# Performance work log

Measured on AMD Instinct MI355X. Metric: run time of the kernel, lower is better.

The kernel has to match this reference:

```python
import jax, jax.numpy as jnp
import numpy as np
from jax import lax

NUM_HEADS = 8
EMBED_DIM = 256
KEY_DIM = EMBED_DIM // NUM_HEADS  # 32


def rotate_every_two(x):
    x1 = x[..., ::2]
    x2 = x[..., 1::2]
    return jnp.stack((-x2, x1), axis=-1).reshape(x.shape)


def theta_shift(x, sin, cos):
    return x * cos + rotate_every_two(x) * sin


def setup_inputs() -> dict:
    key = jax.random.key(0)
    ks = jax.random.split(key, 16)
    b, H, W, E = 16, 64, 64, EMBED_DIM
    kd = KEY_DIM
    gain = 2 ** (-2.5)
    std_proj = gain * (2.0 / (E + E)) ** 0.5  # xavier_normal with gain
    std_out = (2.0 / (E + E)) ** 0.5
    return {
        "x": jax.random.normal(ks[0], (b, H, W, E), jnp.float32),
        "sin": jax.random.normal(ks[1], (H, W, kd), jnp.float32),
        "cos": jax.random.normal(ks[2], (H, W, kd), jnp.float32),
        "mask_h": jax.random.normal(ks[3], (NUM_HEADS, H, H), jnp.float32),
        "mask_w": jax.random.normal(ks[4], (NUM_HEADS, W, W), jnp.float32),
        "q_w": jax.random.normal(ks[5], (E, E), jnp.float32) * std_proj,
        "q_b": jnp.zeros((E,), jnp.float32),
        "k_w": jax.random.normal(ks[6], (E, E), jnp.float32) * std_proj,
        "k_b": jnp.zeros((E,), jnp.float32),
        "v_w": jax.random.normal(ks[7], (E, E), jnp.float32) * std_proj,
        "v_b": jnp.zeros((E,), jnp.float32),
        "lepe_w": jax.random.normal(ks[8], (5, 5, 1, E), jnp.float32) * 0.05,  # HWIO depthwise
        "lepe_b": jnp.zeros((E,), jnp.float32),
        "out_w": jax.random.normal(ks[9], (E, E), jnp.float32) * std_out,
        "out_b": jnp.zeros((E,), jnp.float32),
    }


def reference(x, sin, cos, mask_h, mask_w, q_w, q_b, k_w, k_b, v_w, v_b,
              lepe_w, lepe_b, out_w, out_b):
    b, H, W, E = x.shape
    nH, kd = NUM_HEADS, KEY_DIM
    vd = E // nH
    scaling = kd ** (-0.5)

    q = x @ q_w + q_b                       # [b,H,W,E]
    k = (x @ k_w + k_b) * scaling
    v = x @ v_w + v_b

    # depthwise 5x5 conv (lepe), NHWC
    lepe = lax.conv_general_dilated(
        v, lepe_w, window_strides=(1, 1), padding=[(2, 2), (2, 2)],
        dimension_numbers=("NHWC", "HWIO", "NHWC"), feature_group_count=E) + lepe_b

    q = q.reshape(b, H, W, nH, kd)
    k = k.reshape(b, H, W, nH, kd)
    v = v.reshape(b, H, W, nH, vd)

    sin_b = sin[:, :, None, :]              # [H,W,1,kd]
    cos_b = cos[:, :, None, :]
    qr = theta_shift(q, sin_b, cos_b)       # [b,H,W,nH,kd]
    kr = theta_shift(k, sin_b, cos_b)

    # width-wise attention: scores [b,H,nH,W,W]
    qk_w = jnp.einsum("bhqnd,bhknd->bhnqk", qr, kr)
    attn_w = jax.nn.softmax(qk_w + mask_w[None, None], axis=-1)
    v1 = jnp.einsum("bhnqk,bhknd->bhqnd", attn_w, v)  # [b,H,W,nH,vd]

    # height-wise attention: scores [b,W,nH,H,H]
    qk_h = jnp.einsum("bqwnd,bkwnd->bwnqk", qr, kr)
    attn_h = jax.nn.softmax(qk_h + mask_h[None, None], axis=-1)
    out = jnp.einsum("bwnqk,bkwnd->bqwnd", attn_h, v1)  # [b,H,W,nH,vd]

    out = out.reshape(b, H, W, E) + lepe
    return out @ out_w + out_b
```

## Files before the change

kernel.cpp:

```cpp
#include <hip/hip_runtime.h>

typedef unsigned short u16;
typedef __attribute__((ext_vector_type(4))) float f32x4;
typedef __attribute__((ext_vector_type(8))) short bf16x8;
typedef __attribute__((ext_vector_type(8))) u16 u16x8;
typedef __attribute__((ext_vector_type(4))) u16 u16x4v;

#define DI __device__ __forceinline__

DI u16 f2bf(float f) {
  unsigned int x = __float_as_uint(f);
  unsigned int r = (x + 0x7fffu + ((x >> 16) & 1u)) >> 16;
  return (u16)r;
}
DI float bf2f(u16 u) { return __uint_as_float(((unsigned int)u) << 16); }

__global__ __launch_bounds__(256) void pack_kernel(
    const float* __restrict__ qw, const float* __restrict__ qb,
    const float* __restrict__ kw, const float* __restrict__ kb,
    const float* __restrict__ vw, const float* __restrict__ vb,
    const float* __restrict__ ow,
    u16* __restrict__ wqkvT, float* __restrict__ bias, u16* __restrict__ owT)
{
  const int r = blockIdx.x;
  const int t = threadIdx.x;
  if (r < 768) {
    const int p = r >> 8, c = r & 255;
    const float* wsrc = p == 0 ? qw : (p == 1 ? kw : vw);
    const float sc = (p == 1) ? 0.17677669529663687f : 1.0f;
    wqkvT[r * 256 + t] = f2bf(wsrc[t * 256 + c] * sc);
    if (t == 0) {
      const float* bs = p == 0 ? qb : (p == 1 ? kb : vb);
      bias[r] = bs[c] * sc;
    }
  } else {
    const int c = r - 768;
    owT[c * 256 + t] = f2bf(ow[t * 256 + c]);
  }
}

__global__ __launch_bounds__(256, 6) void qkv_gemm_kernel(
    const float* __restrict__ x, const u16* __restrict__ wT, const float* __restrict__ bias,
    const float* __restrict__ sinp, const float* __restrict__ cosp,
    u16* __restrict__ qr, u16* __restrict__ kr, u16* __restrict__ v)
{
  __shared__ u16 As[16384];
  __shared__ float Tr[4][2][576];
  const int t = threadIdx.x;
  const int wave = t >> 6, lane = t & 63;
  const int g = lane >> 4, lr = lane & 15;
  const int m0 = blockIdx.x * 64;

  {
    char* Abw = (char*)As;
#pragma unroll
    for (int i = 0; i < 16; ++i) {
      const int c = t + 256 * i;
      const int row = c >> 6, cf = c & 63;
      const float4 xv = *reinterpret_cast<const float4*>(x + (m0 + row) * 256 + cf * 4);
      u16x4v bv;
      bv.x = f2bf(xv.x); bv.y = f2bf(xv.y); bv.z = f2bf(xv.z); bv.w = f2bf(xv.w);
      *reinterpret_cast<u16x4v*>(Abw + row * 512 + ((cf * 8) ^ ((row & 7) << 4))) = bv;
    }
  }
  __syncthreads();

  const char* Ab = (const char*)As;
  const int tl8 = lane >> 2;
  const int c8 = (lane & 3) * 8;

  for (int cg = 0; cg < 6; ++cg) {
    const int c0 = cg * 128;
    f32x4 acc[4][2];
#pragma unroll
    for (int i = 0; i < 4; ++i)
#pragma unroll
      for (int j = 0; j < 2; ++j) acc[i][j] = (f32x4){0.f, 0.f, 0.f, 0.f};

#pragma unroll
    for (int ks = 0; ks < 8; ++ks) {
      bf16x8 af[4], bfr[2];
#pragma unroll
      for (int mt = 0; mt < 4; ++mt) {
        const int rr = mt * 16 + lr;
        const int cb = (ks * 64 + g * 16) ^ ((rr & 7) << 4);
        af[mt] = *reinterpret_cast<const bf16x8*>(Ab + rr * 512 + cb);
      }
#pragma unroll
      for (int nt = 0; nt < 2; ++nt)
        bfr[nt] = *reinterpret_cast<const bf16x8*>(wT + (c0 + wave * 32 + nt * 16 + lr) * 256 + ks * 32 + g * 8);
#pragma unroll
      for (int mt = 0; mt < 4; ++mt)
#pragma unroll
        for (int nt = 0; nt < 2; ++nt)
          acc[mt][nt] = __builtin_amdgcn_mfma_f32_16x16x32_bf16(af[mt], bfr[nt], acc[mt][nt], 0, 0, 0);
    }

    const int colb = c0 + wave * 32;
    const int proj = colb >> 8;
    u16* dst = proj == 0 ? qr : (proj == 1 ? kr : v);
    const int e0 = (colb & 255) + c8;

    float bcv[2];
#pragma unroll
    for (int nt = 0; nt < 2; ++nt) bcv[nt] = bias[colb + nt * 16 + lr];

#pragma unroll
    for (int mt = 0; mt < 4; ++mt) {
      float* Trb = Tr[wave][mt & 1];
#pragma unroll
      for (int nt = 0; nt < 2; ++nt)
#pragma unroll
        for (int j = 0; j < 4; ++j)
          Trb[(g * 4 + j) * 36 + nt * 16 + lr] = acc[mt][nt][j] + bcv[nt];
      asm volatile("s_waitcnt lgkmcnt(0)" ::: "memory");
      const int rb = tl8 * 36 + c8;
      const int tok = m0 + mt * 16 + tl8;
      u16x8 o;
      if (proj < 2) {
        const int pos = tok & 4095;
        const float* sp2 = sinp + pos * 32 + c8;
        const float* cp2 = cosp + pos * 32 + c8;
        {
          const float4 v0 = *reinterpret_cast<const float4*>(Trb + rb);
          const float4 s0 = *reinterpret_cast<const float4*>(sp2);
          const float4 cA = *reinterpret_cast<const float4*>(cp2);
          o[0] = f2bf(v0.x * cA.x - v0.y * s0.x);
          o[1] = f2bf(v0.y * cA.y + v0.x * s0.y);
          o[2] = f2bf(v0.z * cA.z - v0.w * s0.z);
          o[3] = f2bf(v0.w * cA.w + v0.z * s0.w);
        }
        {
          const float4 v1 = *reinterpret_cast<const float4*>(Trb + rb + 4);
          const float4 s1 = *reinterpret_cast<const float4*>(sp2 + 4);
          const float4 cB = *reinterpret_cast<const float4*>(cp2 + 4);
          o[4] = f2bf(v1.x * cB.x - v1.y * s1.x);
          o[5] = f2bf(v1.y * cB.y + v1.x * s1.y);
          o[6] = f2bf(v1.z * cB.z - v1.w * s1.z);
          o[7] = f2bf(v1.w * cB.w + v1.z * s1.w);
        }
      } else {
        const float4 v0 = *reinterpret_cast<const float4*>(Trb + rb);
        const float4 v1 = *reinterpret_cast<const float4*>(Trb + rb + 4);
        o[0] = f2bf(v0.x); o[1] = f2bf(v0.y); o[2] = f2bf(v0.z); o[3] = f2bf(v0.w);
        o[4] = f2bf(v1.x); o[5] = f2bf(v1.y); o[6] = f2bf(v1.z); o[7] = f2bf(v1.w);
      }
      *reinterpret_cast<u16x8*>(dst + tok * 256 + e0) = o;
    }
  }
}

__global__ __launch_bounds__(256, 2) void attn_kernel(
    const u16* __restrict__ qr, const u16* __restrict__ kr, const u16* __restrict__ vsrc,
    const float* __restrict__ mask, u16* __restrict__ dst, const int mode)
{
  __shared__ u16 Pbuf[4][64][72];
  __shared__ u16 Vt[256][80];
  const int t = threadIdx.x;
  const int wave = t >> 6, lane = t & 63;
  const int g = lane >> 4, lr = lane & 15;
  const int b = blockIdx.x >> 6, o = blockIdx.x & 63;
  const int base = (mode == 0) ? (b * 4096 + o * 64) * 256 : (b * 4096 + o) * 256;
  const int ts = (mode == 0) ? 256 : 16384;

#pragma unroll
  for (int i = 0; i < 8; ++i) {
    const int c = t + 256 * i;
    const int tok = c >> 5, ch = c & 31;
    const u16x8 val = *reinterpret_cast<const u16x8*>(vsrc + base + tok * ts + ch * 8);
    const int tc = tok ^ ((ch & 7) * 8);
#pragma unroll
    for (int j = 0; j < 8; ++j) Vt[ch * 8 + j][tc] = val[j];
  }
  __syncthreads();

  for (int hh = 0; hh < 2; ++hh) {
    const int n = wave * 2 + hh;
    bf16x8 qf[4], kf[4];
#pragma unroll
    for (int mt = 0; mt < 4; ++mt) {
      qf[mt] = *reinterpret_cast<const bf16x8*>(qr + base + (mt * 16 + lr) * ts + n * 32 + g * 8);
      kf[mt] = *reinterpret_cast<const bf16x8*>(kr + base + (mt * 16 + lr) * ts + n * 32 + g * 8);
    }
    const f32x4 zero = (f32x4){0.f, 0.f, 0.f, 0.f};
    f32x4 s[4][4];
#pragma unroll
    for (int mt = 0; mt < 4; ++mt)
#pragma unroll
      for (int nt = 0; nt < 4; ++nt)
        s[mt][nt] = __builtin_amdgcn_mfma_f32_16x16x32_bf16(qf[mt], kf[nt], zero, 0, 0, 0);

    const float* mp = mask + n * 4096;
#pragma unroll
    for (int mt = 0; mt < 4; ++mt) {
#pragma unroll
      for (int j = 0; j < 4; ++j) {
        const int r = mt * 16 + g * 4 + j;
#pragma unroll
        for (int nt = 0; nt < 4; ++nt)
          s[mt][nt][j] += mp[r * 64 + nt * 16 + lr];
        float m = fmaxf(fmaxf(s[mt][0][j], s[mt][1][j]), fmaxf(s[mt][2][j], s[mt][3][j]));
        m = fmaxf(m, __shfl_xor(m, 1));
        m = fmaxf(m, __shfl_xor(m, 2));
        m = fmaxf(m, __shfl_xor(m, 4));
        m = fmaxf(m, __shfl_xor(m, 8));
        float sum = 0.f;
#pragma unroll
        for (int nt = 0; nt < 4; ++nt) {
          const float p = __expf(s[mt][nt][j] - m);
          s[mt][nt][j] = p;
          sum += p;
        }
        sum += __shfl_xor(sum, 1);
        sum += __shfl_xor(sum, 2);
        sum += __shfl_xor(sum, 4);
        sum += __shfl_xor(sum, 8);
        const float rs = 1.f / sum;
#pragma unroll
        for (int nt = 0; nt < 4; ++nt)
          Pbuf[wave][r][nt * 16 + lr] = f2bf(s[mt][nt][j] * rs);
      }
    }

    f32x4 oacc[4][2];
#pragma unroll
    for (int mt = 0; mt < 4; ++mt)
#pragma unroll
      for (int nd = 0; nd < 2; ++nd) oacc[mt][nd] = zero;

#pragma unroll
    for (int kt = 0; kt < 2; ++kt) {
      bf16x8 pa[4];
#pragma unroll
      for (int mt = 0; mt < 4; ++mt)
        pa[mt] = *reinterpret_cast<const bf16x8*>(&Pbuf[wave][mt * 16 + lr][kt * 32 + g * 8]);
#pragma unroll
      for (int nd = 0; nd < 2; ++nd) {
        const int dcol = n * 32 + nd * 16 + lr;
        const bf16x8 vb = *reinterpret_cast<const bf16x8*>(
            &Vt[dcol][(kt * 32 + g * 8) ^ (((dcol >> 3) & 7) * 8)]);
#pragma unroll
        for (int mt = 0; mt < 4; ++mt)
          oacc[mt][nd] = __builtin_amdgcn_mfma_f32_16x16x32_bf16(pa[mt], vb, oacc[mt][nd], 0, 0, 0);
      }
    }
#pragma unroll
    for (int mt = 0; mt < 4; ++mt)
#pragma unroll
      for (int nd = 0; nd < 2; ++nd)
#pragma unroll
        for (int j = 0; j < 4; ++j)
          dst[base + (mt * 16 + g * 4 + j) * ts + n * 32 + nd * 16 + lr] = f2bf(oacc[mt][nd][j]);
  }
}

__global__ __launch_bounds__(256) void lepe_kernel(
    const u16* __restrict__ v, const float* __restrict__ cw, const float* __restrict__ cb,
    u16* __restrict__ lepe)
{
  const int t = threadIdx.x;
  const int cg = t & 31, pg = t >> 5;
  const int c0 = cg * 8;
  const int rowi = blockIdx.x >> 1;
  const int w0 = (blockIdx.x & 1) * 32 + pg * 4;
  const int h = rowi & 63;

  float acc[4][8];
#pragma unroll
  for (int p = 0; p < 4; ++p)
#pragma unroll
    for (int j = 0; j < 8; ++j) acc[p][j] = 0.f;

#pragma unroll
  for (int dy = 0; dy < 5; ++dy) {
    const int hh = h + dy - 2;
    if ((unsigned)hh >= 64u) continue;
    const u16* vrow = v + (size_t)(rowi + dy - 2) * 64 * 256 + c0;
    float fin[8][8];
#pragma unroll
    for (int i = 0; i < 8; ++i) {
      const int ww = w0 - 2 + i;
      if ((unsigned)ww < 64u) {
        const u16x8 val = *reinterpret_cast<const u16x8*>(vrow + ww * 256);
#pragma unroll
        for (int j = 0; j < 8; ++j) fin[i][j] = bf2f(val[j]);
      } else {
#pragma unroll
        for (int j = 0; j < 8; ++j) fin[i][j] = 0.f;
      }
    }
#pragma unroll
    for (int dx = 0; dx < 5; ++dx) {
      const float* wp = cw + (dy * 5 + dx) * 256 + c0;
      const float4 wA = *reinterpret_cast<const float4*>(wp);
      const float4 wB = *reinterpret_cast<const float4*>(wp + 4);
      const float wv[8] = {wA.x, wA.y, wA.z, wA.w, wB.x, wB.y, wB.z, wB.w};
#pragma unroll
      for (int p = 0; p < 4; ++p)
#pragma unroll
        for (int j = 0; j < 8; ++j)
          acc[p][j] += fin[p + dx][j] * wv[j];
    }
  }

#pragma unroll
  for (int p = 0; p < 4; ++p) {
    u16x8 r;
#pragma unroll
    for (int j = 0; j < 8; ++j) r[j] = f2bf(acc[p][j] + cb[c0 + j]);
    *reinterpret_cast<u16x8*>(lepe + ((size_t)rowi * 64 + w0 + p) * 256 + c0) = r;
  }
}

__global__ __launch_bounds__(256, 6) void out_gemm_kernel(
    const u16* __restrict__ ao, const u16* __restrict__ lep, const u16* __restrict__ owT,
    const float* __restrict__ ob, float* __restrict__ out)
{
  __shared__ u16 As[16384];
  const int t = threadIdx.x;
  const int wave = t >> 6, lane = t & 63;
  const int g = lane >> 4, lr = lane & 15;
  const int m0 = blockIdx.x * 64;

  char* Abw = (char*)As;
#pragma unroll
  for (int i = 0; i < 8; ++i) {
    const int c = t + 256 * i;
    const int row = c >> 5, bc = (c & 31) << 4;
    const int off = (m0 + row) * 256 + (c & 31) * 8;
    const u16x8 a = *reinterpret_cast<const u16x8*>(ao + off);
    const u16x8 l = *reinterpret_cast<const u16x8*>(lep + off);
    u16x8 s;
#pragma unroll
    for (int j = 0; j < 8; ++j) s[j] = f2bf(bf2f(a[j]) + bf2f(l[j]));
    *reinterpret_cast<u16x8*>(Abw + row * 512 + (bc ^ ((row & 7) << 4))) = s;
  }
  __syncthreads();

  const char* Ab = (const char*)As;
  for (int cg = 0; cg < 2; ++cg) {
    const int c0 = cg * 128 + wave * 32;
    f32x4 acc[4][2];
#pragma unroll
    for (int i = 0; i < 4; ++i)
#pragma unroll
      for (int j = 0; j < 2; ++j) acc[i][j] = (f32x4){0.f, 0.f, 0.f, 0.f};

#pragma unroll
    for (int ks = 0; ks < 8; ++ks) {
      bf16x8 af[4], bfr[2];
#pragma unroll
      for (int mt = 0; mt < 4; ++mt) {
        const int rr = mt * 16 + lr;
        const int cb = (ks * 64 + g * 16) ^ ((rr & 7) << 4);
        af[mt] = *reinterpret_cast<const bf16x8*>(Ab + rr * 512 + cb);
      }
#pragma unroll
      for (int nt = 0; nt < 2; ++nt)
        bfr[nt] = *reinterpret_cast<const bf16x8*>(owT + (c0 + nt * 16 + lr) * 256 + ks * 32 + g * 8);
#pragma unroll
      for (int mt = 0; mt < 4; ++mt)
#pragma unroll
        for (int nt = 0; nt < 2; ++nt)
          acc[mt][nt] = __builtin_amdgcn_mfma_f32_16x16x32_bf16(af[mt], bfr[nt], acc[mt][nt], 0, 0, 0);
    }

#pragma unroll
    for (int mt = 0; mt < 4; ++mt) {
#pragma unroll
      for (int nt = 0; nt < 2; ++nt) {
        const int col = c0 + nt * 16 + lr;
        const float bc2 = ob[col];
#pragma unroll
        for (int j = 0; j < 4; ++j) {
          const int tok = m0 + mt * 16 + g * 4 + j;
          out[tok * 256 + col] = acc[mt][nt][j] + bc2;
        }
      }
    }
  }
}

extern "C" void kernel_launch(void* const* d_in, const int* in_sizes, int n_in,
                              void* d_out, int out_size, void* d_ws, size_t ws_size,
                              hipStream_t stream)
{
  const float* x      = (const float*)d_in[0];
  const float* sinp   = (const float*)d_in[1];
  const float* cosp   = (const float*)d_in[2];
  const float* mask_h = (const float*)d_in[3];
  const float* mask_w = (const float*)d_in[4];
  const float* q_w    = (const float*)d_in[5];
  const float* q_b    = (const float*)d_in[6];
  const float* k_w    = (const float*)d_in[7];
  const float* k_b    = (const float*)d_in[8];
  const float* v_w    = (const float*)d_in[9];
  const float* v_b    = (const float*)d_in[10];
  const float* lepe_w = (const float*)d_in[11];
  const float* lepe_b = (const float*)d_in[12];
  const float* out_w  = (const float*)d_in[13];
  const float* out_b  = (const float*)d_in[14];

  unsigned char* ws = (unsigned char*)d_ws;
  const size_t SZ = 33554432;
  u16* qr    = (u16*)(ws);
  u16* kr    = (u16*)(ws + SZ);
  u16* vv    = (u16*)(ws + 2 * SZ);
  u16* v1    = (u16*)(ws + 3 * SZ);
  u16* lepe  = (u16*)(ws + 4 * SZ);
  u16* wqkvT = (u16*)(ws + 5 * SZ);
  u16* owT   = (u16*)(ws + 5 * SZ + 393216);
  float* bias = (float*)(ws + 5 * SZ + 393216 + 131072);
  u16* attn_out = vv;

  pack_kernel<<<1024, 256, 0, stream>>>(q_w, q_b, k_w, k_b, v_w, v_b, out_w, wqkvT, bias, owT);
  qkv_gemm_kernel<<<1024, 256, 0, stream>>>(x, wqkvT, bias, sinp, cosp, qr, kr, vv);
  lepe_kernel<<<2048, 256, 0, stream>>>(vv, lepe_w, lepe_b, lepe);
  attn_kernel<<<1024, 256, 0, stream>>>(qr, kr, vv, mask_w, v1, 0);
  attn_kernel<<<1024, 256, 0, stream>>>(qr, kr, v1, mask_h, attn_out, 1);
  out_gemm_kernel<<<1024, 256, 0, stream>>>(attn_out, lepe, owT, out_b, (float*)d_out);
}
```

Before: 276.7 us.

## Enlarge QKV GEMM tile to 128 rows with 2x2 wave grid and swizzled epilogue

The QKV projection kernel now handles 128 tokens per block instead of 64. Its four waves form a 2x2 grid, each computing a 64x64 output tile, which raises register-level reuse of the A and B fragments. The epilogue staging buffer uses an XOR swizzle in place of padding, to avoid LDS bank conflicts. The block uses twice the shared memory and more accumulators, so occupancy drops (launch bounds 2), and the grid halves to 512 blocks, which may leave CUs underfilled.

```diff
diff --git a/kernel.cpp b/kernel.cpp
--- a/kernel.cpp
+++ b/kernel.cpp
@@ -39,22 +39,23 @@
   }
 }
 
-__global__ __launch_bounds__(256, 6) void qkv_gemm_kernel(
+__global__ __launch_bounds__(256, 2) void qkv_gemm_kernel(
     const float* __restrict__ x, const u16* __restrict__ wT, const float* __restrict__ bias,
     const float* __restrict__ sinp, const float* __restrict__ cosp,
     u16* __restrict__ qr, u16* __restrict__ kr, u16* __restrict__ v)
 {
-  __shared__ u16 As[16384];
-  __shared__ float Tr[4][2][576];
+  __shared__ u16 As[32768];
+  __shared__ float Tr[4][1024];
   const int t = threadIdx.x;
   const int wave = t >> 6, lane = t & 63;
   const int g = lane >> 4, lr = lane & 15;
-  const int m0 = blockIdx.x * 64;
+  const int wr = wave >> 1, wc = wave & 1;
+  const int m0 = blockIdx.x * 128;
 
   {
     char* Abw = (char*)As;
 #pragma unroll
-    for (int i = 0; i < 16; ++i) {
+    for (int i = 0; i < 32; ++i) {
       const int c = t + 256 * i;
       const int row = c >> 6, cf = c & 63;
       const float4 xv = *reinterpret_cast<const float4*>(x + (m0 + row) * 256 + cf * 4);
@@ -66,86 +67,94 @@
   __syncthreads();
 
   const char* Ab = (const char*)As;
-  const int tl8 = lane >> 2;
-  const int c8 = (lane & 3) * 8;
+  float* Trw = Tr[wave];
+  const int tau = lane >> 3;
+  const int kap = lane & 7;
 
   for (int cg = 0; cg < 6; ++cg) {
     const int c0 = cg * 128;
-    f32x4 acc[4][2];
+    f32x4 acc[4][4];
 #pragma unroll
     for (int i = 0; i < 4; ++i)
 #pragma unroll
-      for (int j = 0; j < 2; ++j) acc[i][j] = (f32x4){0.f, 0.f, 0.f, 0.f};
+      for (int j = 0; j < 4; ++j) acc[i][j] = (f32x4){0.f, 0.f, 0.f, 0.f};
 
 #pragma unroll
     for (int ks = 0; ks < 8; ++ks) {
-      bf16x8 af[4], bfr[2];
+      bf16x8 af[4], bfr[4];
 #pragma unroll
       for (int mt = 0; mt < 4; ++mt) {
-        const int rr = mt * 16 + lr;
+        const int rr = wr * 64 + mt * 16 + lr;
         const int cb = (ks * 64 + g * 16) ^ ((rr & 7) << 4);
         af[mt] = *reinterpret_cast<const bf16x8*>(Ab + rr * 512 + cb);
       }
 #pragma unroll
-      for (int nt = 0; nt < 2; ++nt)
-        bfr[nt] = *reinterpret_cast<const bf16x8*>(wT + (c0 + wave * 32 + nt * 16 + lr) * 256 + ks * 32 + g * 8);
+      for (int nt = 0; nt < 4; ++nt)
+        bfr[nt] = *reinterpret_cast<const bf16x8*>(wT + (c0 + wc * 64 + nt * 16 + lr) * 256 + ks * 32 + g * 8);
 #pragma unroll
       for (int mt = 0; mt < 4; ++mt)
 #pragma unroll
-        for (int nt = 0; nt < 2; ++nt)
+        for (int nt = 0; nt < 4; ++nt)
           acc[mt][nt] = __builtin_amdgcn_mfma_f32_16x16x32_bf16(af[mt], bfr[nt], acc[mt][nt], 0, 0, 0);
     }
 
-    const int colb = c0 + wave * 32;
+    const int colb = c0 + wc * 64;
     const int proj = colb >> 8;
     u16* dst = proj == 0 ? qr : (proj == 1 ? kr : v);
-    const int e0 = (colb & 255) + c8;
-
-    float bcv[2];
-#pragma unroll
-    for (int nt = 0; nt < 2; ++nt) bcv[nt] = bias[colb + nt * 16 + lr];
+    const int e0 = (colb & 255) + kap * 8;
+
+    float bcv[4];
+#pragma unroll
+    for (int nt = 0; nt < 4; ++nt) bcv[nt] = bias[colb + nt * 16 + lr];
 
 #pragma unroll
     for (int mt = 0; mt < 4; ++mt) {
-      float* Trb = Tr[wave][mt & 1];
-#pragma unroll
-      for (int nt = 0; nt < 2; ++nt)
+      const int sigw = (8 * ((g * 4) & 3)) ^ (16 * (g & 1));
+#pragma unroll
+      for (int nt = 0; nt < 4; ++nt)
 #pragma unroll
         for (int j = 0; j < 4; ++j)
-          Trb[(g * 4 + j) * 36 + nt * 16 + lr] = acc[mt][nt][j] + bcv[nt];
+          Trw[(g * 4 + j) * 64 + ((nt * 16 + lr) ^ (8 * j) ^ (16 * (g & 1)))] =
+              acc[mt][nt][j] + bcv[nt];
+      (void)sigw;
       asm volatile("s_waitcnt lgkmcnt(0)" ::: "memory");
-      const int rb = tl8 * 36 + c8;
-      const int tok = m0 + mt * 16 + tl8;
-      u16x8 o;
-      if (proj < 2) {
-        const int pos = tok & 4095;
-        const float* sp2 = sinp + pos * 32 + c8;
-        const float* cp2 = cosp + pos * 32 + c8;
-        {
-          const float4 v0 = *reinterpret_cast<const float4*>(Trb + rb);
-          const float4 s0 = *reinterpret_cast<const float4*>(sp2);
-          const float4 cA = *reinterpret_cast<const float4*>(cp2);
-          o[0] = f2bf(v0.x * cA.x - v0.y * s0.x);
-          o[1] = f2bf(v0.y * cA.y + v0.x * s0.y);
-          o[2] = f2bf(v0.z * cA.z - v0.w * s0.z);
-          o[3] = f2bf(v0.w * cA.w + v0.z * s0.w);
+#pragma unroll
+      for (int r2 = 0; r2 < 2; ++r2) {
+        const int row = tau + 8 * r2;
+        const int sig = (8 * (row & 3)) ^ (16 * ((row >> 2) & 1));
+        const int rb = row * 64 + ((kap * 8) ^ sig);
+        const float4 v0 = *reinterpret_cast<const float4*>(Trw + rb);
+        const float4 v1 = *reinterpret_cast<const float4*>(Trw + rb + 4);
+        const int tok = m0 + wr * 64 + mt * 16 + row;
+        u16x8 o;
+        if (proj < 2) {
+          const int pos = tok & 4095;
+          const int d0 = (kap * 8) & 31;
+          const float* sp2 = sinp + pos * 32 + d0;
+          const float* cp2 = cosp + pos * 32 + d0;
+          {
+            const float4 s0 = *reinterpret_cast<const float4*>(sp2);
+            const float4 cA = *reinterpret_cast<const float4*>(cp2);
+            o[0] = f2bf(v0.x * cA.x - v0.y * s0.x);
+            o[1] = f2bf(v0.y * cA.y + v0.x * s0.y);
+            o[2] = f2bf(v0.z * cA.z - v0.w * s0.z);
+            o[3] = f2bf(v0.w * cA.w + v0.z * s0.w);
+          }
+          {
+            const float4 s1 = *reinterpret_cast<const float4*>(sp2 + 4);
+            const float4 cB = *reinterpret_cast<const float4*>(cp2 + 4);
+            o[4] = f2bf(v1.x * cB.x - v1.y * s1.x);
+            o[5] = f2bf(v1.y * cB.y + v1.x * s1.y);
+            o[6] = f2bf(v1.z * cB.z - v1.w * s1.z);
+            o[7] = f2bf(v1.w * cB.w + v1.z * s1.w);
+          }
+        } else {
+          o[0] = f2bf(v0.x); o[1] = f2bf(v0.y); o[2] = f2bf(v0.z); o[3] = f2bf(v0.w);
+          o[4] = f2bf(v1.x); o[5] = f2bf(v1.y); o[6] = f2bf(v1.z); o[7] = f2bf(v1.w);
         }
-        {
-          const float4 v1 = *reinterpret_cast<const float4*>(Trb + rb + 4);
-          const float4 s1 = *reinterpret_cast<const float4*>(sp2 + 4);
-          const float4 cB = *reinterpret_cast<const float4*>(cp2 + 4);
-          o[4] = f2bf(v1.x * cB.x - v1.y * s1.x);
-          o[5] = f2bf(v1.y * cB.y + v1.x * s1.y);
-          o[6] = f2bf(v1.z * cB.z - v1.w * s1.z);
-          o[7] = f2bf(v1.w * cB.w + v1.z * s1.w);
-        }
-      } else {
-        const float4 v0 = *reinterpret_cast<const float4*>(Trb + rb);
-        const float4 v1 = *reinterpret_cast<const float4*>(Trb + rb + 4);
-        o[0] = f2bf(v0.x); o[1] = f2bf(v0.y); o[2] = f2bf(v0.z); o[3] = f2bf(v0.w);
-        o[4] = f2bf(v1.x); o[5] = f2bf(v1.y); o[6] = f2bf(v1.z); o[7] = f2bf(v1.w);
-      }
-      *reinterpret_cast<u16x8*>(dst + tok * 256 + e0) = o;
+        *reinterpret_cast<u16x8*>(dst + tok * 256 + e0) = o;
+      }
+      asm volatile("s_waitcnt lgkmcnt(0)" ::: "memory");
     }
   }
 }
@@ -414,7 +423,7 @@
   u16* attn_out = vv;
 
   pack_kernel<<<1024, 256, 0, stream>>>(q_w, q_b, k_w, k_b, v_w, v_b, out_w, wqkvT, bias, owT);
-  qkv_gemm_kernel<<<1024, 256, 0, stream>>>(x, wqkvT, bias, sinp, cosp, qr, kr, vv);
+  qkv_gemm_kernel<<<512, 256, 0, stream>>>(x, wqkvT, bias, sinp, cosp, qr, kr, vv);
   lepe_kernel<<<2048, 256, 0, stream>>>(vv, lepe_w, lepe_b, lepe);
   attn_kernel<<<1024, 256, 0, stream>>>(qr, kr, vv, mask_w, v1, 0);
   attn_kernel<<<1024, 256, 0, stream>>>(qr, kr, v1, mask_h, attn_out, 1);
```

Result: faster. 269.1 us (-2.8%).
